# Performance work log

Hardware: AMD Instinct MI355X
Metric: run time of the kernel (lower is better)

The kernel has to match this reference:

```python
import jax, jax.numpy as jnp
import numpy as np

C = 1024
H = 16
EPS = 1e-5

def _layernorm(x, g, b):
    mu = jnp.mean(x, axis=-1, keepdims=True)
    var = jnp.mean(jnp.square(x - mu), axis=-1, keepdims=True)
    return (x - mu) * jax.lax.rsqrt(var + EPS) * g + b

def _mha(xq, xkv, wq, bq, wk, bk, wv, bv, wo, bo, causal):
    B, T, Cm = xq.shape
    Tc = xkv.shape[1]
    d = Cm // H
    q = (xq @ wq + bq).reshape(B, T, H, d)
    k = (xkv @ wk + bk).reshape(B, Tc, H, d)
    v = (xkv @ wv + bv).reshape(B, Tc, H, d)
    att = jnp.einsum('bthd,bshd->bhts', q, k) * (1.0 / np.sqrt(d))
    if causal:
        mask = jnp.tril(jnp.ones((T, Tc), dtype=bool))
        att = jnp.where(mask[None, None], att, -jnp.inf)
    att = jax.nn.softmax(att, axis=-1)
    y = jnp.einsum('bhts,bshd->bthd', att, v).reshape(B, T, Cm)
    return y @ wo + bo


def setup_inputs() -> dict:
    key = jax.random.key(0)
    ks = jax.random.split(key, 20)
    s = 0.02
    w = lambda k: (s * jax.random.normal(k, (C, C))).astype(jnp.float32)
    inp = {
        'x': jax.random.normal(ks[0], (4, 1024, C), dtype=jnp.float32),
        'context': jax.random.normal(ks[1], (4, 1024, C), dtype=jnp.float32),
        'ln1_g': jnp.ones((C,)), 'ln1_b': jnp.zeros((C,)),
        'ln2_g': jnp.ones((C,)), 'ln2_b': jnp.zeros((C,)),
        'sa_wq': w(ks[2]), 'sa_bq': jnp.zeros((C,)),
        'sa_wk': w(ks[3]), 'sa_bk': jnp.zeros((C,)),
        'sa_wv': w(ks[4]), 'sa_bv': jnp.zeros((C,)),
        'sa_wo': w(ks[5]), 'sa_bo': jnp.zeros((C,)),
        'ca_wq': w(ks[6]), 'ca_bq': jnp.zeros((C,)),
        'ca_wk': w(ks[7]), 'ca_bk': jnp.zeros((C,)),
        'ca_wv': w(ks[8]), 'ca_bv': jnp.zeros((C,)),
        'ca_wo': w(ks[9]), 'ca_bo': jnp.zeros((C,)),
        'mlp_w1': (s * jax.random.normal(ks[10], (C, 4 * C))).astype(jnp.float32),
        'mlp_b1': jnp.zeros((4 * C,)),
        'mlp_w2': (s * jax.random.normal(ks[11], (4 * C, C))).astype(jnp.float32),
        'mlp_b2': jnp.zeros((C,)),
    }
    return inp


def reference(x, context, ln1_g, ln1_b, ln2_g, ln2_b,
              sa_wq, sa_bq, sa_wk, sa_bk, sa_wv, sa_bv, sa_wo, sa_bo,
              ca_wq, ca_bq, ca_wk, ca_bk, ca_wv, ca_bv, ca_wo, ca_bo,
              mlp_w1, mlp_b1, mlp_w2, mlp_b2):
    # x = x + self_attn(ln1(x))  (causal)
    x = x + _mha(_layernorm(x, ln1_g, ln1_b), _layernorm(x, ln1_g, ln1_b),
                 sa_wq, sa_bq, sa_wk, sa_bk, sa_wv, sa_bv, sa_wo, sa_bo, causal=True)
    # x = x + cross_attn(ln2(x), context)  (non-causal)
    x = x + _mha(_layernorm(x, ln2_g, ln2_b), context,
                 ca_wq, ca_bq, ca_wk, ca_bk, ca_wv, ca_bv, ca_wo, ca_bo, causal=False)
    # x = x + mlp(ln2(x))  -- note: the module reuses ln2 here (as in source)
    h = _layernorm(x, ln2_g, ln2_b)
    h = jax.nn.gelu(h @ mlp_w1 + mlp_b1, approximate=False) @ mlp_w2 + mlp_b2
    x = x + h
    return x
```

## Files before the change

### kernel.cpp

```cpp
#include <hip/hip_runtime.h>
#include <hip/hip_bf16.h>

typedef __attribute__((ext_vector_type(8))) short s8v;
typedef __attribute__((ext_vector_type(4))) float f4v;

#define DEV static __device__ __forceinline__

DEV unsigned short f2bf(float f) {
    unsigned int u = __builtin_bit_cast(unsigned int, f);
    unsigned int r = u + 0x7FFFu + ((u >> 16) & 1u);
    return (unsigned short)(r >> 16);
}

DEV f4v fzero() { f4v v = {0.f, 0.f, 0.f, 0.f}; return v; }

DEV float fgelu(float x) {
    float z = x * (1.5957691f + 0.07135482f * x * x);
    float s = __builtin_amdgcn_rcpf(1.0f + __expf(-z));
    return x * s;
}

DEV void gload16(const void* g, void* l) {
    __builtin_amdgcn_global_load_lds(
        (const __attribute__((address_space(1))) unsigned int*)g,
        (__attribute__((address_space(3))) unsigned int*)l, 16, 0, 0);
}

struct P8 { const float* p[8]; };
__global__ __launch_bounds__(256) void k_transpose8(
        P8 ws8, unsigned short* __restrict__ base) {
    __shared__ float tile[32][33];
    int z = blockIdx.z;
    const float* W = ws8.p[z];
    unsigned short* Wt = base + (size_t)z * 1024 * 1024;
    int tx = threadIdx.x & 31, ty = threadIdx.x >> 5;
    int n0 = blockIdx.x * 32, k0 = blockIdx.y * 32;
#pragma unroll
    for (int r = 0; r < 32; r += 8)
        tile[ty + r][tx] = W[(size_t)(k0 + ty + r) * 1024 + n0 + tx];
    __syncthreads();
#pragma unroll
    for (int r = 0; r < 32; r += 8)
        Wt[(size_t)(n0 + ty + r) * 1024 + k0 + tx] = f2bf(tile[tx][ty + r]);
}

__global__ __launch_bounds__(256) void k_transpose_bf16(
        const float* __restrict__ W, unsigned short* __restrict__ Wt, int K, int N) {
    __shared__ float tile[32][33];
    int tx = threadIdx.x & 31, ty = threadIdx.x >> 5;
    int n0 = blockIdx.x * 32, k0 = blockIdx.y * 32;
#pragma unroll
    for (int r = 0; r < 32; r += 8)
        tile[ty + r][tx] = W[(size_t)(k0 + ty + r) * N + n0 + tx];
    __syncthreads();
#pragma unroll
    for (int r = 0; r < 32; r += 8)
        Wt[(size_t)(n0 + ty + r) * K + k0 + tx] = f2bf(tile[tx][ty + r]);
}

__global__ __launch_bounds__(256) void k_f32_to_bf16(
        const float* __restrict__ in, unsigned short* __restrict__ out, int n) {
    int i = (blockIdx.x * 256 + threadIdx.x) * 8;
    if (i >= n) return;
    float4 a = *(const float4*)(in + i);
    float4 b = *(const float4*)(in + i + 4);
    uint4 o;
    o.x = f2bf(a.x) | ((unsigned)f2bf(a.y) << 16);
    o.y = f2bf(a.z) | ((unsigned)f2bf(a.w) << 16);
    o.z = f2bf(b.x) | ((unsigned)f2bf(b.y) << 16);
    o.w = f2bf(b.z) | ((unsigned)f2bf(b.w) << 16);
    *(uint4*)(out + i) = o;
}

__global__ __launch_bounds__(256) void k_bias_cat(
        const float* q, const float* k, const float* v,
        const float* k2, const float* v2, float* out) {
    int i = blockIdx.x * 256 + threadIdx.x;
    float val;
    if (i < 1024) val = q[i];
    else if (i < 2048) val = k[i - 1024];
    else if (i < 3072) val = v[i - 2048];
    else if (i < 4096) val = k2[i - 3072];
    else val = v2[i - 4096];
    out[i] = val;
}

__global__ __launch_bounds__(256) void k_layernorm(
        const float* __restrict__ x, const float* __restrict__ g,
        const float* __restrict__ b, unsigned short* __restrict__ out) {
    int row = blockIdx.x;
    int t = threadIdx.x;
    const float* xr = x + (size_t)row * 1024;
    float4 v = *(const float4*)(xr + t * 4);
    float s = v.x + v.y + v.z + v.w;
    float ss = v.x * v.x + v.y * v.y + v.z * v.z + v.w * v.w;
#pragma unroll
    for (int m = 1; m < 64; m <<= 1) { s += __shfl_xor(s, m); ss += __shfl_xor(ss, m); }
    __shared__ float red[16];
    int w = t >> 6;
    if ((t & 63) == 0) { red[w] = s; red[8 + w] = ss; }
    __syncthreads();
    s = red[0] + red[1] + red[2] + red[3];
    ss = red[8] + red[9] + red[10] + red[11];
    float mu = s * (1.f / 1024.f);
    float rstd = rsqrtf(ss * (1.f / 1024.f) - mu * mu + 1e-5f);
    float4 gv = *(const float4*)(g + t * 4);
    float4 bv = *(const float4*)(b + t * 4);
    float y0 = (v.x - mu) * rstd * gv.x + bv.x;
    float y1 = (v.y - mu) * rstd * gv.y + bv.y;
    float y2 = (v.z - mu) * rstd * gv.z + bv.z;
    float y3 = (v.w - mu) * rstd * gv.w + bv.w;
    uint2 o;
    o.x = f2bf(y0) | ((unsigned)f2bf(y1) << 16);
    o.y = f2bf(y2) | ((unsigned)f2bf(y3) << 16);
    *(uint2*)(out + (size_t)row * 1024 + t * 4) = o;
}

template <int EPI, int BM>
__global__ __launch_bounds__(256) void k_gemm(
        const unsigned short* __restrict__ A, const unsigned short* __restrict__ Bt,
        const float* __restrict__ bias, const float* __restrict__ res,
        void* __restrict__ outv, int M, int N, int K) {
    constexpr int WI = (BM == 128) ? 4 : 2;
    constexpr int ABUF = BM * 64;
    constexpr int BUFSZ = ABUF + 8192;
    constexpr int LPT = (BM == 128) ? 4 : 3;
    __shared__ __align__(16) char smem[3 * BUFSZ];
    int nbx = N >> 7;
    int bid = blockIdx.x;
    int cpx = gridDim.x >> 3;
    int swz = (bid & 7) * cpx + (bid >> 3);
    int bx = swz % nbx, by = swz / nbx;
    int m0 = by * BM, n0 = bx << 7;
    int tid = threadIdx.x, w = tid >> 6, l = tid & 63;
    int wr = w >> 1, wc = w & 1;
    int lq = l >> 4, lc = l & 15;
    f4v acc[WI][4];
#pragma unroll
    for (int i = 0; i < WI; ++i)
#pragma unroll
        for (int j = 0; j < 4; ++j) acc[i][j] = fzero();
    const unsigned short* Ab = A + (size_t)m0 * K;
    const unsigned short* Bb = Bt + (size_t)n0 * K;
    int arow = w * 16 + (l >> 2);
    int ach = (((l & 3) ^ ((arow >> 1) & 3)) << 3);

    auto STAGE = [&](int t) {
        int kt = t << 5;
        char* buf = smem + (t % 3) * BUFSZ;
        gload16(Ab + (size_t)arow * K + kt + ach, buf + w * 1024);
        if constexpr (BM == 128)
            gload16(Ab + (size_t)(64 + arow) * K + kt + ach, buf + 4096 + w * 1024);
        gload16(Bb + (size_t)arow * K + kt + ach, buf + ABUF + w * 1024);
        gload16(Bb + (size_t)(64 + arow) * K + kt + ach, buf + ABUF + 4096 + w * 1024);
    };
    int cs = ((lq ^ ((lc >> 1) & 3)) << 4);
    auto COMPUTE = [&](int t) {
        const char* buf = smem + (t % 3) * BUFSZ;
        s8v af[WI], bfr[4];
#pragma unroll
        for (int i = 0; i < WI; ++i)
            af[i] = *(const s8v*)(buf + (wr * (BM / 2) + i * 16 + lc) * 64 + cs);
#pragma unroll
        for (int j = 0; j < 4; ++j)
            bfr[j] = *(const s8v*)(buf + ABUF + (wc * 64 + j * 16 + lc) * 64 + cs);
#pragma unroll
        for (int i = 0; i < WI; ++i)
#pragma unroll
            for (int j = 0; j < 4; ++j)
                acc[i][j] = __builtin_amdgcn_mfma_f32_16x16x32_bf16(af[i], bfr[j], acc[i][j], 0, 0, 0);
    };

    int NT = K >> 5;
    STAGE(0); STAGE(1);
    if constexpr (BM == 128) asm volatile("s_waitcnt vmcnt(4)" ::: "memory");
    else                     asm volatile("s_waitcnt vmcnt(3)" ::: "memory");
    __builtin_amdgcn_s_barrier();
    for (int t = 0; t < NT; ++t) {
        if (t + 2 < NT) STAGE(t + 2);
        COMPUTE(t);
        if (t + 2 < NT) {
            if constexpr (BM == 128) asm volatile("s_waitcnt vmcnt(4)" ::: "memory");
            else                     asm volatile("s_waitcnt vmcnt(3)" ::: "memory");
        } else if (t + 1 < NT) {
            asm volatile("s_waitcnt vmcnt(0)" ::: "memory");
        }
        __builtin_amdgcn_s_barrier();
    }

    float* esc = (float*)smem + w * 1088;
#pragma unroll
    for (int i = 0; i < WI; ++i) {
#pragma unroll
        for (int j = 0; j < 4; ++j)
#pragma unroll
            for (int r = 0; r < 4; ++r)
                esc[(lq * 4 + r) * 68 + j * 16 + lc] = acc[i][j][r];
#pragma unroll
        for (int p = 0; p < 4; ++p) {
            int rr = p * 4 + lq;
            float4 v = *(const float4*)(esc + rr * 68 + lc * 4);
            int row = m0 + wr * (BM / 2) + i * 16 + rr;
            int col = n0 + wc * 64 + lc * 4;
            float4 bv = *(const float4*)(bias + col);
            v.x += bv.x; v.y += bv.y; v.z += bv.z; v.w += bv.w;
            size_t idx = (size_t)row * N + col;
            if (EPI == 0) {
                ushort4 o;
                o.x = f2bf(v.x); o.y = f2bf(v.y); o.z = f2bf(v.z); o.w = f2bf(v.w);
                *(ushort4*)((unsigned short*)outv + idx) = o;
            } else if (EPI == 1) {
                ushort4 o;
                o.x = f2bf(fgelu(v.x)); o.y = f2bf(fgelu(v.y));
                o.z = f2bf(fgelu(v.z)); o.w = f2bf(fgelu(v.w));
                *(ushort4*)((unsigned short*)outv + idx) = o;
            } else {
                float4 rv = *(const float4*)(res + idx);
                v.x += rv.x; v.y += rv.y; v.z += rv.z; v.w += rv.w;
                *(float4*)((float*)outv + idx) = v;
            }
        }
    }
}

__global__ __launch_bounds__(256) void k_attn(
        const unsigned short* __restrict__ Q, int ldq,
        const unsigned short* __restrict__ Kp, int ldk,
        const unsigned short* __restrict__ Vp, int ldv,
        unsigned short* __restrict__ O, int ldo,
        int T, int causal) {
    __shared__ unsigned short Ks[64 * 64];
    __shared__ unsigned short Vt[64 * 64];
    __shared__ unsigned short Ps[4][16 * 64];
    int nqt = T >> 6;
    int qt = blockIdx.x % nqt;
    int bh = blockIdx.x / nqt;
    int b = bh >> 4, h = bh & 15;
    int tid = threadIdx.x, w = tid >> 6, l = tid & 63;
    int lq = l >> 4, lc = l & 15;
    size_t qoff = (size_t)b * T * ldq + h * 64;
    size_t koff = (size_t)b * T * ldk + h * 64;
    size_t voff = (size_t)b * T * ldv + h * 64;
    s8v qf[2];
    {
        const unsigned short* qp = Q + qoff + (size_t)(qt * 64 + w * 16 + lc) * ldq + lq * 8;
        qf[0] = *(const s8v*)qp;
        qf[1] = *(const s8v*)(qp + 32);
    }
    f4v o_acc[4];
#pragma unroll
    for (int j = 0; j < 4; ++j) o_acc[j] = fzero();
    float mrow[4], lrow[4];
#pragma unroll
    for (int j = 0; j < 4; ++j) { mrow[j] = -3.0e38f; lrow[j] = 0.f; }
    int p = tid & 31, dbase = (tid >> 5) * 8;
    int ktend = causal ? (qt + 1) : (T >> 6);
    for (int kt = 0; kt < ktend; ++kt) {
#pragma unroll
        for (int s = 0; s < 2; ++s) {
            int idx = s * 256 + w * 64 + l;
            int t = idx >> 3;
            int ch = (idx & 7) ^ (t & 7);
            gload16(Kp + koff + (size_t)(kt * 64 + t) * ldk + ch * 8,
                    (char*)Ks + s * 4096 + w * 1024);
        }
        {
            const unsigned short* vp = Vp + voff + (size_t)(kt * 64 + 2 * p) * ldv + dbase;
            s8v v0 = *(const s8v*)vp;
            s8v v1 = *(const s8v*)(vp + ldv);
#pragma unroll
            for (int j = 0; j < 8; ++j) {
                int dd = dbase + j;
                unsigned int val = (unsigned short)v0[j] | ((unsigned)(unsigned short)v1[j] << 16);
                *(unsigned int*)((char*)Vt + dd * 128 +
                                 ((((p >> 2) ^ (dd & 7)) << 4) | ((p & 3) << 2))) = val;
            }
        }
        __syncthreads();
        f4v sa[4];
#pragma unroll
        for (int jn = 0; jn < 4; ++jn) {
            sa[jn] = fzero();
            int t = jn * 16 + lc;
#pragma unroll
            for (int kc = 0; kc < 2; ++kc) {
                s8v bf = *(const s8v*)((const char*)Ks + t * 128 +
                                       (((kc * 4 + lq) ^ (t & 7)) << 4));
                sa[jn] = __builtin_amdgcn_mfma_f32_16x16x32_bf16(qf[kc], bf, sa[jn], 0, 0, 0);
            }
        }
        bool diag = (causal && kt == qt);
#pragma unroll
        for (int j = 0; j < 4; ++j) {
            float pv[4];
            float tm = -3.0e38f;
#pragma unroll
            for (int jn = 0; jn < 4; ++jn) {
                float sv = sa[jn][j] * 0.125f;
                if (diag) {
                    int qg = w * 16 + lq * 4 + j;
                    int kg = jn * 16 + lc;
                    if (kg > qg) sv = -3.0e38f;
                }
                pv[jn] = sv;
                tm = fmaxf(tm, sv);
            }
#pragma unroll
            for (int m = 1; m < 16; m <<= 1) tm = fmaxf(tm, __shfl_xor(tm, m));
            float mnew = fmaxf(mrow[j], tm);
            float alpha = __expf(mrow[j] - mnew);
            mrow[j] = mnew;
            float rs = 0.f;
#pragma unroll
            for (int jn = 0; jn < 4; ++jn) {
                float e = __expf(pv[jn] - mnew);
                rs += e;
                int colx = jn * 16 + lc;
                int rowx = lq * 4 + j;
                *(unsigned short*)((char*)Ps[w] + rowx * 128 +
                                   ((((colx >> 3) ^ (rowx & 7)) << 4) | ((colx & 7) << 1))) = f2bf(e);
            }
#pragma unroll
            for (int m = 1; m < 16; m <<= 1) rs += __shfl_xor(rs, m);
            lrow[j] = lrow[j] * alpha + rs;
#pragma unroll
            for (int jn = 0; jn < 4; ++jn) o_acc[jn][j] *= alpha;
        }
#pragma unroll
        for (int kc = 0; kc < 2; ++kc) {
            s8v af = *(const s8v*)((const char*)Ps[w] + lc * 128 +
                                   (((kc * 4 + lq) ^ (lc & 7)) << 4));
#pragma unroll
            for (int jn = 0; jn < 4; ++jn) {
                int dd = jn * 16 + lc;
                s8v bf = *(const s8v*)((const char*)Vt + dd * 128 +
                                       (((kc * 4 + lq) ^ (dd & 7)) << 4));
                o_acc[jn] = __builtin_amdgcn_mfma_f32_16x16x32_bf16(af, bf, o_acc[jn], 0, 0, 0);
            }
        }
        __syncthreads();
    }
#pragma unroll
    for (int j = 0; j < 4; ++j) {
        float inv = 1.0f / lrow[j];
        int row = qt * 64 + w * 16 + lq * 4 + j;
#pragma unroll
        for (int jn = 0; jn < 4; ++jn)
            O[(size_t)(b * T + row) * ldo + h * 64 + jn * 16 + lc] = f2bf(o_acc[jn][j] * inv);
    }
}

extern "C" void kernel_launch(void* const* d_in, const int* in_sizes, int n_in,
                              void* d_out, int out_size, void* d_ws, size_t ws_size,
                              hipStream_t stream) {
    const float* x     = (const float*)d_in[0];
    const float* ctx   = (const float*)d_in[1];
    const float* ln1_g = (const float*)d_in[2];
    const float* ln1_b = (const float*)d_in[3];
    const float* ln2_g = (const float*)d_in[4];
    const float* ln2_b = (const float*)d_in[5];
    const float* sa_wq = (const float*)d_in[6];  const float* sa_bq = (const float*)d_in[7];
    const float* sa_wk = (const float*)d_in[8];  const float* sa_bk = (const float*)d_in[9];
    const float* sa_wv = (const float*)d_in[10]; const float* sa_bv = (const float*)d_in[11];
    const float* sa_wo = (const float*)d_in[12]; const float* sa_bo = (const float*)d_in[13];
    const float* ca_wq = (const float*)d_in[14]; const float* ca_bq = (const float*)d_in[15];
    const float* ca_wk = (const float*)d_in[16]; const float* ca_bk = (const float*)d_in[17];
    const float* ca_wv = (const float*)d_in[18]; const float* ca_bv = (const float*)d_in[19];
    const float* ca_wo = (const float*)d_in[20]; const float* ca_bo = (const float*)d_in[21];
    const float* w1 = (const float*)d_in[22]; const float* b1 = (const float*)d_in[23];
    const float* w2 = (const float*)d_in[24]; const float* b2 = (const float*)d_in[25];
    float* out = (float*)d_out;

    char* ws = (char*)d_ws;
    const size_t MB = 1024 * 1024;
    unsigned short* wt_base = (unsigned short*)(ws + 0 * MB);
    unsigned short* wt_saq = wt_base + 0 * 1024 * 1024;
    unsigned short* wt_cak = wt_base + 5 * 1024 * 1024;
    unsigned short* wt_sao = wt_base + 3 * 1024 * 1024;
    unsigned short* wt_caq = wt_base + 4 * 1024 * 1024;
    unsigned short* wt_cao = wt_base + 7 * 1024 * 1024;
    unsigned short* w1t    = (unsigned short*)(ws + 16 * MB);
    unsigned short* w2t    = (unsigned short*)(ws + 24 * MB);
    unsigned short* ctxb   = (unsigned short*)(ws + 32 * MB);
    float*          x1     = (float*)        (ws + 40 * MB);
    unsigned short* qbuf   = (unsigned short*)(ws + 56 * MB);
    unsigned short* kbuf   = (unsigned short*)(ws + 64 * MB);
    unsigned short* hln    = (unsigned short*)(ws + 80 * MB);
    float*          bcat   = (float*)        (ws + 88 * MB);
    unsigned short* qkv = qbuf;
    unsigned short* kv  = kbuf;
    unsigned short* m1  = qbuf;
    unsigned short* h3  = ctxb;

    dim3 blk(256);
    P8 ws8;
    ws8.p[0] = sa_wq; ws8.p[1] = sa_wk; ws8.p[2] = sa_wv; ws8.p[3] = sa_wo;
    ws8.p[4] = ca_wq; ws8.p[5] = ca_wk; ws8.p[6] = ca_wv; ws8.p[7] = ca_wo;
    k_transpose8<<<dim3(32, 32, 8), blk, 0, stream>>>(ws8, wt_base);
    k_transpose_bf16<<<dim3(128, 32), blk, 0, stream>>>(w1, w1t, 1024, 4096);
    k_transpose_bf16<<<dim3(32, 128), blk, 0, stream>>>(w2, w2t, 4096, 1024);
    k_f32_to_bf16<<<dim3(2048), blk, 0, stream>>>(ctx, ctxb, 4 * 1024 * 1024);
    k_bias_cat<<<dim3(20), blk, 0, stream>>>(sa_bq, sa_bk, sa_bv, ca_bk, ca_bv, bcat);

    k_layernorm<<<dim3(4096), blk, 0, stream>>>(x, ln1_g, ln1_b, hln);
    k_gemm<0, 128><<<dim3(24 * 32), blk, 0, stream>>>(hln, wt_saq, bcat, nullptr, qkv, 4096, 3072, 1024);
    k_attn<<<dim3(1024), blk, 0, stream>>>(qkv, 3072, qkv + 1024, 3072, qkv + 2048, 3072,
                                           hln, 1024, 1024, 1);
    k_gemm<2, 64><<<dim3(64 * 8), blk, 0, stream>>>(hln, wt_sao, sa_bo, x, x1, 4096, 1024, 1024);

    k_layernorm<<<dim3(4096), blk, 0, stream>>>(x1, ln2_g, ln2_b, hln);
    k_gemm<0, 64><<<dim3(64 * 8), blk, 0, stream>>>(hln, wt_caq, ca_bq, nullptr, qbuf, 4096, 1024, 1024);
    k_gemm<0, 128><<<dim3(16 * 32), blk, 0, stream>>>(ctxb, wt_cak, bcat + 3072, nullptr, kv, 4096, 2048, 1024);
    k_attn<<<dim3(1024), blk, 0, stream>>>(qbuf, 1024, kv, 2048, kv + 1024, 2048,
                                           hln, 1024, 1024, 0);
    k_gemm<2, 64><<<dim3(64 * 8), blk, 0, stream>>>(hln, wt_cao, ca_bo, x1, out, 4096, 1024, 1024);

    k_layernorm<<<dim3(4096), blk, 0, stream>>>(out, ln2_g, ln2_b, h3);
    k_gemm<1, 128><<<dim3(32 * 32), blk, 0, stream>>>(h3, w1t, b1, nullptr, m1, 4096, 4096, 1024);
    k_gemm<2, 64><<<dim3(64 * 8), blk, 0, stream>>>(m1, w2t, b2, out, out, 4096, 1024, 4096);
}
```

Before: 378.3 us.

## Pair causal query tiles per block and compute row sums via MFMA

After: 359.9 us. -4.9%, faster.

```diff
diff --git a/kernel.cpp b/kernel.cpp
--- a/kernel.cpp
+++ b/kernel.cpp
@@ -124,7 +124,6 @@
     constexpr int WI = (BM == 128) ? 4 : 2;
     constexpr int ABUF = BM * 64;
     constexpr int BUFSZ = ABUF + 8192;
-    constexpr int LPT = (BM == 128) ? 4 : 3;
     __shared__ __align__(16) char smem[3 * BUFSZ];
     int nbx = N >> 7;
     int bid = blockIdx.x;
@@ -223,73 +222,59 @@
     }
 }
 
+template <bool CAUSAL>
 __global__ __launch_bounds__(256) void k_attn(
         const unsigned short* __restrict__ Q, int ldq,
         const unsigned short* __restrict__ Kp, int ldk,
         const unsigned short* __restrict__ Vp, int ldv,
-        unsigned short* __restrict__ O, int ldo,
-        int T, int causal) {
+        unsigned short* __restrict__ O, int ldo, int T) {
     __shared__ unsigned short Ks[64 * 64];
     __shared__ unsigned short Vt[64 * 64];
     __shared__ unsigned short Ps[4][16 * 64];
     int nqt = T >> 6;
-    int qt = blockIdx.x % nqt;
-    int bh = blockIdx.x / nqt;
+    int qt0, qt1, bh;
+    if (CAUSAL) {
+        int pairs = nqt >> 1;
+        int pr = blockIdx.x % pairs;
+        bh = blockIdx.x / pairs;
+        qt0 = pr; qt1 = nqt - 1 - pr;
+    } else {
+        qt1 = blockIdx.x % nqt;
+        bh = blockIdx.x / nqt;
+        qt0 = 0;
+    }
     int b = bh >> 4, h = bh & 15;
     int tid = threadIdx.x, w = tid >> 6, l = tid & 63;
     int lq = l >> 4, lc = l & 15;
     size_t qoff = (size_t)b * T * ldq + h * 64;
     size_t koff = (size_t)b * T * ldk + h * 64;
     size_t voff = (size_t)b * T * ldv + h * 64;
-    s8v qf[2];
+    s8v qf1[2], qf0[2];
     {
-        const unsigned short* qp = Q + qoff + (size_t)(qt * 64 + w * 16 + lc) * ldq + lq * 8;
-        qf[0] = *(const s8v*)qp;
-        qf[1] = *(const s8v*)(qp + 32);
-    }
-    f4v o_acc[4];
-#pragma unroll
-    for (int j = 0; j < 4; ++j) o_acc[j] = fzero();
-    float mrow[4], lrow[4];
-#pragma unroll
-    for (int j = 0; j < 4; ++j) { mrow[j] = -3.0e38f; lrow[j] = 0.f; }
+        const unsigned short* qp = Q + qoff + (size_t)(qt1 * 64 + w * 16 + lc) * ldq + lq * 8;
+        qf1[0] = *(const s8v*)qp;
+        qf1[1] = *(const s8v*)(qp + 32);
+        if (CAUSAL) {
+            const unsigned short* q0p = Q + qoff + (size_t)(qt0 * 64 + w * 16 + lc) * ldq + lq * 8;
+            qf0[0] = *(const s8v*)q0p;
+            qf0[1] = *(const s8v*)(q0p + 32);
+        }
+    }
+    s8v ones;
+#pragma unroll
+    for (int i = 0; i < 8; ++i) ones[i] = (short)0x3F80;
+    f4v o1[4], o0[4];
+    float m1r[4], l1r[4], m0r[4], l0r[4];
+#pragma unroll
+    for (int j = 0; j < 4; ++j) {
+        o1[j] = fzero(); o0[j] = fzero();
+        m1r[j] = -3.0e38f; l1r[j] = 0.f; m0r[j] = -3.0e38f; l0r[j] = 0.f;
+    }
     int p = tid & 31, dbase = (tid >> 5) * 8;
-    int ktend = causal ? (qt + 1) : (T >> 6);
-    for (int kt = 0; kt < ktend; ++kt) {
-#pragma unroll
-        for (int s = 0; s < 2; ++s) {
-            int idx = s * 256 + w * 64 + l;
-            int t = idx >> 3;
-            int ch = (idx & 7) ^ (t & 7);
-            gload16(Kp + koff + (size_t)(kt * 64 + t) * ldk + ch * 8,
-                    (char*)Ks + s * 4096 + w * 1024);
-        }
-        {
-            const unsigned short* vp = Vp + voff + (size_t)(kt * 64 + 2 * p) * ldv + dbase;
-            s8v v0 = *(const s8v*)vp;
-            s8v v1 = *(const s8v*)(vp + ldv);
-#pragma unroll
-            for (int j = 0; j < 8; ++j) {
-                int dd = dbase + j;
-                unsigned int val = (unsigned short)v0[j] | ((unsigned)(unsigned short)v1[j] << 16);
-                *(unsigned int*)((char*)Vt + dd * 128 +
-                                 ((((p >> 2) ^ (dd & 7)) << 4) | ((p & 3) << 2))) = val;
-            }
-        }
-        __syncthreads();
-        f4v sa[4];
-#pragma unroll
-        for (int jn = 0; jn < 4; ++jn) {
-            sa[jn] = fzero();
-            int t = jn * 16 + lc;
-#pragma unroll
-            for (int kc = 0; kc < 2; ++kc) {
-                s8v bf = *(const s8v*)((const char*)Ks + t * 128 +
-                                       (((kc * 4 + lq) ^ (t & 7)) << 4));
-                sa[jn] = __builtin_amdgcn_mfma_f32_16x16x32_bf16(qf[kc], bf, sa[jn], 0, 0, 0);
-            }
-        }
-        bool diag = (causal && kt == qt);
+
+    auto SMPV = [&](f4v (&sa)[4], f4v (&oa)[4], float (&mr)[4], float (&lr)[4],
+                    int qt, int kt) {
+        bool diag = CAUSAL && kt == qt;
 #pragma unroll
         for (int j = 0; j < 4; ++j) {
             float pv[4];
@@ -307,46 +292,108 @@
             }
 #pragma unroll
             for (int m = 1; m < 16; m <<= 1) tm = fmaxf(tm, __shfl_xor(tm, m));
-            float mnew = fmaxf(mrow[j], tm);
-            float alpha = __expf(mrow[j] - mnew);
-            mrow[j] = mnew;
-            float rs = 0.f;
+            float mnew = fmaxf(mr[j], tm);
+            float alpha = __expf(mr[j] - mnew);
+            mr[j] = mnew;
 #pragma unroll
             for (int jn = 0; jn < 4; ++jn) {
                 float e = __expf(pv[jn] - mnew);
-                rs += e;
-                int colx = jn * 16 + lc;
-                int rowx = lq * 4 + j;
+                int colx = jn * 16 + lc, rowx = lq * 4 + j;
                 *(unsigned short*)((char*)Ps[w] + rowx * 128 +
                                    ((((colx >> 3) ^ (rowx & 7)) << 4) | ((colx & 7) << 1))) = f2bf(e);
             }
-#pragma unroll
-            for (int m = 1; m < 16; m <<= 1) rs += __shfl_xor(rs, m);
-            lrow[j] = lrow[j] * alpha + rs;
-#pragma unroll
-            for (int jn = 0; jn < 4; ++jn) o_acc[jn][j] *= alpha;
-        }
+            lr[j] *= alpha;
+#pragma unroll
+            for (int jn = 0; jn < 4; ++jn) oa[jn][j] *= alpha;
+        }
+        f4v sone = fzero();
 #pragma unroll
         for (int kc = 0; kc < 2; ++kc) {
             s8v af = *(const s8v*)((const char*)Ps[w] + lc * 128 +
                                    (((kc * 4 + lq) ^ (lc & 7)) << 4));
+            sone = __builtin_amdgcn_mfma_f32_16x16x32_bf16(af, ones, sone, 0, 0, 0);
 #pragma unroll
             for (int jn = 0; jn < 4; ++jn) {
                 int dd = jn * 16 + lc;
                 s8v bf = *(const s8v*)((const char*)Vt + dd * 128 +
                                        (((kc * 4 + lq) ^ (dd & 7)) << 4));
-                o_acc[jn] = __builtin_amdgcn_mfma_f32_16x16x32_bf16(af, bf, o_acc[jn], 0, 0, 0);
+                oa[jn] = __builtin_amdgcn_mfma_f32_16x16x32_bf16(af, bf, oa[jn], 0, 0, 0);
+            }
+        }
+#pragma unroll
+        for (int j = 0; j < 4; ++j) lr[j] += sone[j];
+    };
+
+    int ktend = CAUSAL ? (qt1 + 1) : nqt;
+    for (int kt = 0; kt < ktend; ++kt) {
+#pragma unroll
+        for (int s = 0; s < 2; ++s) {
+            int idx = s * 256 + w * 64 + l;
+            int t = idx >> 3;
+            int ch = (idx & 7) ^ (t & 7);
+            gload16(Kp + koff + (size_t)(kt * 64 + t) * ldk + ch * 8,
+                    (char*)Ks + s * 4096 + w * 1024);
+        }
+        {
+            const unsigned short* vp = Vp + voff + (size_t)(kt * 64 + 2 * p) * ldv + dbase;
+            s8v v0 = *(const s8v*)vp;
+            s8v v1 = *(const s8v*)(vp + ldv);
+#pragma unroll
+            for (int j = 0; j < 8; ++j) {
+                int dd = dbase + j;
+                unsigned int val = (unsigned short)v0[j] | ((unsigned)(unsigned short)v1[j] << 16);
+                *(unsigned int*)((char*)Vt + dd * 128 +
+                                 ((((p >> 2) ^ (dd & 7)) << 4) | ((p & 3) << 2))) = val;
             }
         }
         __syncthreads();
+        bool do0 = CAUSAL && (kt <= qt0);
+        f4v sa1[4], sa0[4];
+#pragma unroll
+        for (int jn = 0; jn < 4; ++jn) {
+            sa1[jn] = fzero();
+            int t = jn * 16 + lc;
+#pragma unroll
+            for (int kc = 0; kc < 2; ++kc) {
+                s8v bf = *(const s8v*)((const char*)Ks + t * 128 +
+                                       (((kc * 4 + lq) ^ (t & 7)) << 4));
+                sa1[jn] = __builtin_amdgcn_mfma_f32_16x16x32_bf16(qf1[kc], bf, sa1[jn], 0, 0, 0);
+            }
+        }
+        if (do0) {
+#pragma unroll
+            for (int jn = 0; jn < 4; ++jn) {
+                sa0[jn] = fzero();
+                int t = jn * 16 + lc;
+#pragma unroll
+                for (int kc = 0; kc < 2; ++kc) {
+                    s8v bf = *(const s8v*)((const char*)Ks + t * 128 +
+                                           (((kc * 4 + lq) ^ (t & 7)) << 4));
+                    sa0[jn] = __builtin_amdgcn_mfma_f32_16x16x32_bf16(qf0[kc], bf, sa0[jn], 0, 0, 0);
+                }
+            }
+        }
+        SMPV(sa1, o1, m1r, l1r, qt1, kt);
+        if (do0) SMPV(sa0, o0, m0r, l0r, qt0, kt);
+        __syncthreads();
     }
 #pragma unroll
     for (int j = 0; j < 4; ++j) {
-        float inv = 1.0f / lrow[j];
-        int row = qt * 64 + w * 16 + lq * 4 + j;
+        float inv = 1.0f / l1r[j];
+        int row = qt1 * 64 + w * 16 + lq * 4 + j;
 #pragma unroll
         for (int jn = 0; jn < 4; ++jn)
-            O[(size_t)(b * T + row) * ldo + h * 64 + jn * 16 + lc] = f2bf(o_acc[jn][j] * inv);
+            O[(size_t)(b * T + row) * ldo + h * 64 + jn * 16 + lc] = f2bf(o1[jn][j] * inv);
+    }
+    if (CAUSAL) {
+#pragma unroll
+        for (int j = 0; j < 4; ++j) {
+            float inv = 1.0f / l0r[j];
+            int row = qt0 * 64 + w * 16 + lq * 4 + j;
+#pragma unroll
+            for (int jn = 0; jn < 4; ++jn)
+                O[(size_t)(b * T + row) * ldo + h * 64 + jn * 16 + lc] = f2bf(o0[jn][j] * inv);
+        }
     }
 }
 
@@ -404,15 +451,15 @@
 
     k_layernorm<<<dim3(4096), blk, 0, stream>>>(x, ln1_g, ln1_b, hln);
     k_gemm<0, 128><<<dim3(24 * 32), blk, 0, stream>>>(hln, wt_saq, bcat, nullptr, qkv, 4096, 3072, 1024);
-    k_attn<<<dim3(1024), blk, 0, stream>>>(qkv, 3072, qkv + 1024, 3072, qkv + 2048, 3072,
-                                           hln, 1024, 1024, 1);
+    k_attn<true><<<dim3(512), blk, 0, stream>>>(qkv, 3072, qkv + 1024, 3072, qkv + 2048, 3072,
+                                                hln, 1024, 1024);
     k_gemm<2, 64><<<dim3(64 * 8), blk, 0, stream>>>(hln, wt_sao, sa_bo, x, x1, 4096, 1024, 1024);
 
     k_layernorm<<<dim3(4096), blk, 0, stream>>>(x1, ln2_g, ln2_b, hln);
     k_gemm<0, 64><<<dim3(64 * 8), blk, 0, stream>>>(hln, wt_caq, ca_bq, nullptr, qbuf, 4096, 1024, 1024);
     k_gemm<0, 128><<<dim3(16 * 32), blk, 0, stream>>>(ctxb, wt_cak, bcat + 3072, nullptr, kv, 4096, 2048, 1024);
-    k_attn<<<dim3(1024), blk, 0, stream>>>(qbuf, 1024, kv, 2048, kv + 1024, 2048,
-                                           hln, 1024, 1024, 0);
+    k_attn<false><<<dim3(1024), blk, 0, stream>>>(qbuf, 1024, kv, 2048, kv + 1024, 2048,
+                                                  hln, 1024, 1024);
     k_gemm<2, 64><<<dim3(64 * 8), blk, 0, stream>>>(hln, wt_cao, ca_bo, x1, out, 4096, 1024, 1024);
 
     k_layernorm<<<dim3(4096), blk, 0, stream>>>(out, ln2_g, ln2_b, h3);
```
